# Performance work log

Hardware: AMD Instinct MI355X
Metric: run time of the kernel (lower is better)

The kernel has to match this reference:

```python
import jax, jax.numpy as jnp
import numpy as np

BITS = 8
CLIP_BOUND = 2.0 ** (BITS - 1) - 1.0  # 127 for int8
EPS = 1e-12


def _per_tensor_scale(x):
    # Dynamic per-tensor abs-max calibration (TensorQuantizer.update with
    # calibration over the whole tensor): scale maps abs-max to the clip bound.
    amax = jnp.max(jnp.abs(x))
    return CLIP_BOUND / jnp.maximum(amax, EPS)


def setup_inputs() -> dict:
    key = jax.random.key(0)
    k1, k2 = jax.random.split(key)
    lhs = jax.random.normal(k1, (4096, 4096), dtype=jnp.float32)
    rhs = jax.random.normal(k2, (4096, 4096), dtype=jnp.float32)
    return {"lhs": lhs, "rhs": rhs}


def reference(lhs, rhs):
    # --- calibration (scales are statistics, no gradient flows through them) ---
    ls = _per_tensor_scale(lhs)
    rs = _per_tensor_scale(rhs)

    # --- quantize to int8 grid ---
    ql = jnp.clip(jnp.round(lhs * ls), -CLIP_BOUND, CLIP_BOUND).astype(jnp.int8)
    qr = jnp.clip(jnp.round(rhs * rs), -CLIP_BOUND, CLIP_BOUND).astype(jnp.int8)

    # --- integer dot_general with int32 accumulation (aqt_dot_general core) ---
    dimension_numbers = (((1,), (0,)), ((), ()))
    acc = jax.lax.dot_general(
        ql, qr, dimension_numbers, preferred_element_type=jnp.int32
    )

    # --- dequantize by product of scales ---
    out = acc.astype(jnp.float32) / (ls * rs)
    return out
```

## Files before the change

### kernel.cpp

```cpp
#include <hip/hip_runtime.h>
#include <stdint.h>


#define NROW 4096
#define NELEM (4096 * 4096)

typedef __attribute__((ext_vector_type(4))) int int32x4;
typedef __attribute__((ext_vector_type(16))) int int32x16;
typedef const __attribute__((address_space(1))) int8_t* gptr1_t;
typedef __attribute__((address_space(3))) int8_t* lptr3_t;

__global__ void absmax_both_kernel(const float* __restrict__ lhs,
                                   const float* __restrict__ rhs,
                                   unsigned* __restrict__ amax) {
    __shared__ float red[4];
    const int t = blockIdx.x & 1;
    const float4* x4 = (const float4*)(t ? rhs : lhs);
    const int bid = blockIdx.x >> 1;
    const int stride = (gridDim.x >> 1) * blockDim.x;
    int i = bid * blockDim.x + threadIdx.x;
    float m0 = 0.0f, m1 = 0.0f, m2 = 0.0f, m3 = 0.0f;
    for (; i + 3 * stride < NELEM / 4; i += 4 * stride) {
        float4 a = x4[i];
        float4 b = x4[i + stride];
        float4 c = x4[i + 2 * stride];
        float4 d = x4[i + 3 * stride];
        m0 = fmaxf(m0, fmaxf(fmaxf(fabsf(a.x), fabsf(a.y)),
                             fmaxf(fabsf(a.z), fabsf(a.w))));
        m1 = fmaxf(m1, fmaxf(fmaxf(fabsf(b.x), fabsf(b.y)),
                             fmaxf(fabsf(b.z), fabsf(b.w))));
        m2 = fmaxf(m2, fmaxf(fmaxf(fabsf(c.x), fabsf(c.y)),
                             fmaxf(fabsf(c.z), fabsf(c.w))));
        m3 = fmaxf(m3, fmaxf(fmaxf(fabsf(d.x), fabsf(d.y)),
                             fmaxf(fabsf(d.z), fabsf(d.w))));
    }
    for (; i < NELEM / 4; i += stride) {
        float4 a = x4[i];
        m0 = fmaxf(m0, fmaxf(fmaxf(fabsf(a.x), fabsf(a.y)),
                             fmaxf(fabsf(a.z), fabsf(a.w))));
    }
    float m = fmaxf(fmaxf(m0, m1), fmaxf(m2, m3));
    for (int off = 32; off > 0; off >>= 1)
        m = fmaxf(m, __shfl_down(m, off, 64));
    const int lane = threadIdx.x & 63, wave = threadIdx.x >> 6;
    if (lane == 0) red[wave] = m;
    __syncthreads();
    if (threadIdx.x == 0) {
        float b = fmaxf(fmaxf(red[0], red[1]), fmaxf(red[2], red[3]));
        atomicMax(amax + t, __float_as_uint(b));
    }
}

__device__ __forceinline__ int q8(float v, float s) {
    int r = __float2int_rn(v * s);
    r = r < -127 ? -127 : r;
    r = r > 127 ? 127 : r;
    return r;
}

__device__ __forceinline__ int pack4(float a, float b, float c, float d,
                                     float s) {
    return (q8(a, s) & 0xff) | ((q8(b, s) & 0xff) << 8) |
           ((q8(c, s) & 0xff) << 16) | ((q8(d, s) & 0xff) << 24);
}

__global__ void quant_kernel(const float* __restrict__ lhs,
                             const float* __restrict__ rhs,
                             int8_t* __restrict__ qA, int8_t* __restrict__ qT,
                             const unsigned* __restrict__ amax) {
    __shared__ int8_t sm[64][68];
    if (blockIdx.x < 4096) {
        const float s = 127.0f / fmaxf(__uint_as_float(amax[0]), 1e-12f);
        const int c = blockIdx.x * 256 + threadIdx.x;
        const int l = c & 63;
        const int ks_g = (c >> 6) & 127;
        const int mt_g = c >> 13;
        const int row = mt_g * 32 + (l & 31);
        const int kb = ks_g * 32 + (l >> 5) * 16;
        const float4* src = (const float4*)(lhs + (size_t)row * NROW + kb);
        float4 v0 = src[0], v1 = src[1], v2 = src[2], v3 = src[3];
        int4 w;
        w.x = pack4(v0.x, v0.y, v0.z, v0.w, s);
        w.y = pack4(v1.x, v1.y, v1.z, v1.w, s);
        w.z = pack4(v2.x, v2.y, v2.z, v2.w, s);
        w.w = pack4(v3.x, v3.y, v3.z, v3.w, s);
        *(int4*)(qA + (size_t)c * 16) = w;
    } else {
        const float s = 127.0f / fmaxf(__uint_as_float(amax[1]), 1e-12f);
        const int b = blockIdx.x - 4096;
        const int n0 = (b & 63) * 64, k0 = (b >> 6) * 64;
        const int rl = threadIdx.x >> 4;
        const int nq = threadIdx.x & 15;
        for (int r = 0; r < 4; ++r) {
            const int kl = r * 16 + rl;
            float4 v = *(const float4*)(rhs + (size_t)(k0 + kl) * NROW + n0 + nq * 4);
            sm[nq * 4 + 0][kl] = (int8_t)q8(v.x, s);
            sm[nq * 4 + 1][kl] = (int8_t)q8(v.y, s);
            sm[nq * 4 + 2][kl] = (int8_t)q8(v.z, s);
            sm[nq * 4 + 3][kl] = (int8_t)q8(v.w, s);
        }
        __syncthreads();
        const int nt_l = threadIdx.x >> 7;
        const int ks_l = (threadIdx.x >> 6) & 1;
        const int l = threadIdx.x & 63;
        const int n_loc = nt_l * 32 + (l & 31);
        const int k_loc = ks_l * 32 + (l >> 5) * 16;
        int4 w;
        w.x = *(const int*)&sm[n_loc][k_loc + 0];
        w.y = *(const int*)&sm[n_loc][k_loc + 4];
        w.z = *(const int*)&sm[n_loc][k_loc + 8];
        w.w = *(const int*)&sm[n_loc][k_loc + 12];
        const int nt_g = (b & 63) * 2 + nt_l;
        const int ks_g = (b >> 6) * 2 + ks_l;
        *(int4*)(qT + (((size_t)nt_g * 128 + ks_g) * 64 + l) * 16) = w;
    }
}

__global__ __launch_bounds__(512, 2) void gemm_i8_kernel(
    const int8_t* __restrict__ qA, const int8_t* __restrict__ qBT,
    float* __restrict__ out, const unsigned* __restrict__ amax) {
    __shared__ __align__(16) int8_t sA[2][32768];
    __shared__ __align__(16) int8_t sB[2][32768];

    const int tid = threadIdx.x;
    const int lane = tid & 63;
    const int wave = tid >> 6;
    const int wm = wave >> 2;
    const int wn = wave & 3;

    const int bid = blockIdx.y * 16 + blockIdx.x;
    const int swz = (bid & 7) * 32 + (bid >> 3);
    const int m0 = (swz >> 4) * 256, n0 = (swz & 15) * 256;

    const int rl = lane & 31;
    const int hi = lane >> 5;

    const gptr1_t pA0 = (gptr1_t)(qA + (size_t)(m0 / 32 + (tid >> 8)) * 131072 +
                                  (tid & 255) * 16);
    const gptr1_t pB0 = (gptr1_t)(qBT + (size_t)(n0 / 32 + (tid >> 8)) * 131072 +
                                  (tid & 255) * 16);
    int8_t* sAf = &sA[0][0];
    int8_t* sBf = &sB[0][0];
    const int dst0 = tid * 16;

    auto stage = [&](int slot, int kt) {
        const int kb = kt * 4096;
#pragma unroll
        for (int j = 0; j < 4; ++j) {
            __builtin_amdgcn_global_load_lds(
                pA0 + (size_t)j * 262144 + kb,
                (lptr3_t)(sAf + slot * 32768 + dst0 + j * 8192), 16, 0, 0);
            __builtin_amdgcn_global_load_lds(
                pB0 + (size_t)j * 262144 + kb,
                (lptr3_t)(sBf + slot * 32768 + dst0 + j * 8192), 16, 0, 0);
        }
    };

    int32x16 acc[4][2];
#pragma unroll
    for (int mt = 0; mt < 4; ++mt)
#pragma unroll
        for (int nt = 0; nt < 2; ++nt) acc[mt][nt] = (int32x16)(0);

    const int aBase = wm * 16384 + lane * 16;
    const int bBase = wn * 8192 + lane * 16;

    auto compute = [&](const int8_t* a, const int8_t* b) {
#pragma unroll
        for (int ks = 0; ks < 4; ++ks) {
            int32x4 af[4], bf[2];
#pragma unroll
            for (int mt = 0; mt < 4; ++mt)
                af[mt] = *(const int32x4*)(a + aBase + mt * 4096 + ks * 1024);
#pragma unroll
            for (int nt = 0; nt < 2; ++nt)
                bf[nt] = *(const int32x4*)(b + bBase + nt * 4096 + ks * 1024);
            __builtin_amdgcn_s_setprio(1);
#pragma unroll
            for (int mt = 0; mt < 4; ++mt)
#pragma unroll
                for (int nt = 0; nt < 2; ++nt)
                    acc[mt][nt] = __builtin_amdgcn_mfma_i32_32x32x32_i8(
                        af[mt], bf[nt], acc[mt][nt], 0, 0, 0);
            __builtin_amdgcn_s_setprio(0);
        }
    };

    stage(0, 0);
    asm volatile("s_waitcnt vmcnt(0)" ::: "memory");
    __builtin_amdgcn_sched_barrier(0);
    __builtin_amdgcn_s_barrier();
    __builtin_amdgcn_sched_barrier(0);

#pragma unroll 1
    for (int w = 0; w < 31; ++w) {
        stage((w + 1) & 1, w + 1);
        compute(sAf + (w & 1) * 32768, sBf + (w & 1) * 32768);
        asm volatile("s_waitcnt vmcnt(0)" ::: "memory");
        __builtin_amdgcn_sched_barrier(0);
        __builtin_amdgcn_s_barrier();
        __builtin_amdgcn_sched_barrier(0);
    }
    compute(sAf + 32768, sBf + 32768);

    const float ls = 127.0f / fmaxf(__uint_as_float(amax[0]), 1e-12f);
    const float rs = 127.0f / fmaxf(__uint_as_float(amax[1]), 1e-12f);
    const float inv = 1.0f / (ls * rs);
#pragma unroll
    for (int mt = 0; mt < 4; ++mt)
#pragma unroll
        for (int nt = 0; nt < 2; ++nt)
#pragma unroll
            for (int reg = 0; reg < 16; ++reg) {
                const int row = m0 + wm * 128 + mt * 32 + (reg & 3) +
                                8 * (reg >> 2) + 4 * hi;
                const int col = n0 + wn * 64 + nt * 32 + rl;
                out[(size_t)row * NROW + col] = (float)acc[mt][nt][reg] * inv;
            }
}

extern "C" void kernel_launch(void* const* d_in, const int* in_sizes, int n_in,
                              void* d_out, int out_size, void* d_ws,
                              size_t ws_size, hipStream_t stream) {
    const float* lhs = (const float*)d_in[0];
    const float* rhs = (const float*)d_in[1];
    float* out = (float*)d_out;

    int8_t* qA = (int8_t*)d_ws;
    int8_t* qBT = qA + (size_t)16 * 1024 * 1024;
    unsigned* amax = (unsigned*)(qBT + (size_t)16 * 1024 * 1024);

    hipMemsetAsync(amax, 0, 8, stream);
    absmax_both_kernel<<<2048, 256, 0, stream>>>(lhs, rhs, amax);
    quant_kernel<<<4096 + 4096, 256, 0, stream>>>(lhs, rhs, qA, qBT, amax);
    gemm_i8_kernel<<<dim3(16, 16), 512, 0, stream>>>(qA, qBT, out, amax);
}
```

Measured before the change: 137.1 us.

## Load B fragments directly from global into registers, bypassing LDS

Drops the shared-memory staging buffer for the B operand. Each wave now loads its B MFMA fragments straight from the pre-swizzled global layout into registers, double-buffered across half k-steps, and the wait relaxes to vmcnt(4). This halves LDS footprint and LDS traffic, which may allow higher occupancy and fewer LDS reads. In exchange, B data is no longer shared across the waves in a block (the wm=0/1 waves load the same B), so L2/global traffic goes up and register pressure rises.

```diff
diff --git a/kernel.cpp b/kernel.cpp
--- a/kernel.cpp
+++ b/kernel.cpp
@@ -120,7 +120,6 @@
     const int8_t* __restrict__ qA, const int8_t* __restrict__ qBT,
     float* __restrict__ out, const unsigned* __restrict__ amax) {
     __shared__ __align__(16) int8_t sA[2][32768];
-    __shared__ __align__(16) int8_t sB[2][32768];
 
     const int tid = threadIdx.x;
     const int lane = tid & 63;
@@ -137,10 +136,7 @@
 
     const gptr1_t pA0 = (gptr1_t)(qA + (size_t)(m0 / 32 + (tid >> 8)) * 131072 +
                                   (tid & 255) * 16);
-    const gptr1_t pB0 = (gptr1_t)(qBT + (size_t)(n0 / 32 + (tid >> 8)) * 131072 +
-                                  (tid & 255) * 16);
     int8_t* sAf = &sA[0][0];
-    int8_t* sBf = &sB[0][0];
     const int dst0 = tid * 16;
 
     auto stage = [&](int slot, int kt) {
@@ -150,12 +146,11 @@
             __builtin_amdgcn_global_load_lds(
                 pA0 + (size_t)j * 262144 + kb,
                 (lptr3_t)(sAf + slot * 32768 + dst0 + j * 8192), 16, 0, 0);
-            __builtin_amdgcn_global_load_lds(
-                pB0 + (size_t)j * 262144 + kb,
-                (lptr3_t)(sBf + slot * 32768 + dst0 + j * 8192), 16, 0, 0);
         }
     };
 
+    const int8_t* pbW = qBT + (size_t)(n0 / 32 + wn * 2) * 131072 + lane * 16;
+
     int32x16 acc[4][2];
 #pragma unroll
     for (int mt = 0; mt < 4; ++mt)
@@ -163,30 +158,37 @@
         for (int nt = 0; nt < 2; ++nt) acc[mt][nt] = (int32x16)(0);
 
     const int aBase = wm * 16384 + lane * 16;
-    const int bBase = wn * 8192 + lane * 16;
-
-    auto compute = [&](const int8_t* a, const int8_t* b) {
-#pragma unroll
-        for (int ks = 0; ks < 4; ++ks) {
-            int32x4 af[4], bf[2];
-#pragma unroll
-            for (int mt = 0; mt < 4; ++mt)
-                af[mt] = *(const int32x4*)(a + aBase + mt * 4096 + ks * 1024);
-#pragma unroll
-            for (int nt = 0; nt < 2; ++nt)
-                bf[nt] = *(const int32x4*)(b + bBase + nt * 4096 + ks * 1024);
-            __builtin_amdgcn_s_setprio(1);
-#pragma unroll
-            for (int mt = 0; mt < 4; ++mt)
-#pragma unroll
-                for (int nt = 0; nt < 2; ++nt)
-                    acc[mt][nt] = __builtin_amdgcn_mfma_i32_32x32x32_i8(
-                        af[mt], bf[nt], acc[mt][nt], 0, 0, 0);
-            __builtin_amdgcn_s_setprio(0);
-        }
-    };
+
+    int32x4 B0[4], B1[4];
+
+#define LOADB(B, KT, KS0)                                                     \
+    {                                                                         \
+        const int8_t* bp = pbW + (size_t)(KT)*4096 + (KS0)*1024;              \
+        B[0] = *(const int32x4*)(bp);                                         \
+        B[1] = *(const int32x4*)(bp + 1024);                                  \
+        B[2] = *(const int32x4*)(bp + 131072);                                \
+        B[3] = *(const int32x4*)(bp + 131072 + 1024);                         \
+    }
+
+#define HALF(APTR, B, KS0)                                                    \
+    {                                                                         \
+        _Pragma("unroll") for (int k = 0; k < 2; ++k) {                       \
+            int32x4 af[4];                                                    \
+            _Pragma("unroll") for (int mt = 0; mt < 4; ++mt) af[mt] =         \
+                *(const int32x4*)((APTR) + aBase + mt * 4096 +                \
+                                  ((KS0) + k) * 1024);                        \
+            __builtin_amdgcn_s_setprio(1);                                    \
+            _Pragma("unroll") for (int mt = 0; mt < 4; ++mt)                  \
+                _Pragma("unroll") for (int nt = 0; nt < 2; ++nt)              \
+                    acc[mt][nt] = __builtin_amdgcn_mfma_i32_32x32x32_i8(      \
+                        af[mt], B[nt * 2 + k], acc[mt][nt], 0, 0, 0);         \
+            __builtin_amdgcn_s_setprio(0);                                    \
+        }                                                                     \
+    }
 
     stage(0, 0);
+    __builtin_amdgcn_sched_barrier(0);
+    LOADB(B0, 0, 0)
     asm volatile("s_waitcnt vmcnt(0)" ::: "memory");
     __builtin_amdgcn_sched_barrier(0);
     __builtin_amdgcn_s_barrier();
@@ -194,14 +196,24 @@
 
 #pragma unroll 1
     for (int w = 0; w < 31; ++w) {
+        const int8_t* a = sAf + (w & 1) * 32768;
         stage((w + 1) & 1, w + 1);
-        compute(sAf + (w & 1) * 32768, sBf + (w & 1) * 32768);
-        asm volatile("s_waitcnt vmcnt(0)" ::: "memory");
+        __builtin_amdgcn_sched_barrier(0);
+        LOADB(B1, w, 2)
+        HALF(a, B0, 0)
+        LOADB(B0, w + 1, 0)
+        HALF(a, B1, 2)
+        asm volatile("s_waitcnt vmcnt(4)" ::: "memory");
         __builtin_amdgcn_sched_barrier(0);
         __builtin_amdgcn_s_barrier();
         __builtin_amdgcn_sched_barrier(0);
     }
-    compute(sAf + 32768, sBf + 32768);
+    {
+        const int8_t* a = sAf + 32768;
+        LOADB(B1, 31, 2)
+        HALF(a, B0, 0)
+        HALF(a, B1, 2)
+    }
 
     const float ls = 127.0f / fmaxf(__uint_as_float(amax[0]), 1e-12f);
     const float rs = 127.0f / fmaxf(__uint_as_float(amax[1]), 1e-12f);
@@ -217,6 +229,8 @@
                 const int col = n0 + wn * 64 + nt * 32 + rl;
                 out[(size_t)row * NROW + col] = (float)acc[mt][nt][reg] * inv;
             }
+#undef LOADB
+#undef HALF
 }
 
 extern "C" void kernel_launch(void* const* d_in, const int* in_sizes, int n_in,
```

Result: slower. 142.8 us (+4.1%).
